# Performance work log

Measured on AMD Instinct MI355X. Metric: run time of the kernel, lower is better.

Reference implementation:

```python
import jax, jax.numpy as jnp
import numpy as np

E = 8           # num_local_experts
H = 1024        # hidden_size
F = 1024        # moe_ffn_hidden_size (per-half; fc1 out = 2*F due to GLU)
T = 16384       # total dispatched tokens
GLU_LINEAR_OFFSET = 1.0


def setup_inputs() -> dict:
    key = jax.random.key(0)
    ks = jax.random.split(key, 7)
    s1 = 1.0 / np.sqrt(H)
    s2 = 1.0 / np.sqrt(F)
    return {
        "hidden_states": jax.random.normal(ks[0], (T, H), jnp.float32),
        "tokens_per_expert": jnp.full((E,), T // E, dtype=jnp.int64),
        "probs": jax.random.uniform(ks[1], (T,), jnp.float32),
        # expert params; torch Linear W is [out,in], stored here as [in,out] (same math)
        "W1": jax.random.uniform(ks[2], (E, H, 2 * F), jnp.float32, -s1, s1),
        "b1": jax.random.uniform(ks[3], (E, 2 * F), jnp.float32, -s1, s1),
        "W2": jax.random.uniform(ks[4], (E, F, H), jnp.float32, -s2, s2),
        "b2": jax.random.uniform(ks[5], (E, H), jnp.float32, -s2, s2),
    }


def reference(hidden_states, tokens_per_expert, probs, W1, b1, W2, b2):
    # Tokens arrive grouped contiguously by expert with equal counts (as in
    # setup_inputs), so the split/loop/cat in the torch module is exactly a
    # reshape + grouped (batched) GEMM over the expert axis.
    e = W1.shape[0]
    t, h = hidden_states.shape
    x = hidden_states.reshape(e, t // e, h)            # [E, Tpe, H]
    p = probs.reshape(e, t // e)                       # [E, Tpe]
    # fc1 (gated)
    y = jnp.einsum('eth,ehf->etf', x, W1) + b1[:, None, :]  # [E, Tpe, 2F]
    gate, lin = jnp.split(y, 2, axis=-1)
    a = jax.nn.silu(gate) * (lin + GLU_LINEAR_OFFSET)       # [E, Tpe, F]
    a = a * p[..., None]                                    # per-token scale
    # fc2
    out = jnp.einsum('etf,efh->eth', a, W2) + b2[:, None, :]
    return out.reshape(t, h)
```

## Files before the change

### kernel.cpp

```cpp
#include <hip/hip_runtime.h>
#include <hip/hip_bf16.h>
#include <stdint.h>

#define T_TOK 16384
#define H_DIM 1024
#define F_DIM 1024
#define E_NUM 8
#define TPE   2048

typedef unsigned short u16;
typedef __attribute__((ext_vector_type(8))) short bf16x8;
typedef __attribute__((ext_vector_type(4))) float f32x4;
typedef __attribute__((ext_vector_type(8))) u16 u16x8;

__device__ __forceinline__ u16 f2bf(float x) {
  unsigned int u = __float_as_uint(x);
  u = (u + 0x7fffu + ((u >> 16) & 1u)) >> 16;
  return (u16)u;
}

#define GLD16(gp, lp)                                                          \
  __builtin_amdgcn_global_load_lds(                                            \
      (const __attribute__((address_space(1))) void*)(gp),                     \
      (__attribute__((address_space(3))) void*)(lp), 16, 0, 0)

__global__ __launch_bounds__(256) void prep_all(
    const float* __restrict__ x, const float* __restrict__ W1,
    const float* __restrict__ W2, u16* __restrict__ xbf,
    u16* __restrict__ w1t, u16* __restrict__ w2t) {
  const int bid = blockIdx.x;
  const int t = threadIdx.x;

  if (bid < 4096) {
    size_t base = (size_t)bid * 4096 + (size_t)t * 16;
    const float4* s = (const float4*)(x + base);
    float4 v0 = s[0], v1 = s[1], v2 = s[2], v3 = s[3];
    u16x8 o0, o1;
    o0[0] = f2bf(v0.x); o0[1] = f2bf(v0.y); o0[2] = f2bf(v0.z); o0[3] = f2bf(v0.w);
    o0[4] = f2bf(v1.x); o0[5] = f2bf(v1.y); o0[6] = f2bf(v1.z); o0[7] = f2bf(v1.w);
    o1[0] = f2bf(v2.x); o1[1] = f2bf(v2.y); o1[2] = f2bf(v2.z); o1[3] = f2bf(v2.w);
    o1[4] = f2bf(v3.x); o1[5] = f2bf(v3.y); o1[6] = f2bf(v3.z); o1[7] = f2bf(v3.w);
    *(u16x8*)(xbf + base) = o0;
    *(u16x8*)(xbf + base + 8) = o1;
    return;
  }

  const float* src; u16* dst; int R, C, gw;
  int e, rc, cc;
  const int lane = t & 63;
  const int wid = t >> 6;
  if (bid < 6144) {
    src = W1; dst = w1t; R = H_DIM; C = 2 * F_DIM;
    gw = (bid - 4096) * 4 + wid;
    e = gw >> 10; int rem = gw & 1023; rc = rem >> 5; cc = rem & 31;
  } else {
    src = W2; dst = w2t; R = F_DIM; C = H_DIM;
    gw = (bid - 6144) * 4 + wid;
    e = gw >> 9; int rem = gw & 511; rc = rem >> 4; cc = rem & 15;
  }
  const int row0 = rc << 5;
  const int col0 = cc << 6;
  const float* s = src + (size_t)e * R * C + (size_t)row0 * C + col0 + lane;
  float v[32];
#pragma unroll
  for (int r = 0; r < 32; ++r) v[r] = s[(size_t)r * C];
  u16* d = dst + (size_t)e * C * R + (size_t)(col0 + lane) * R + row0;
#pragma unroll
  for (int k = 0; k < 4; ++k) {
    u16x8 w;
#pragma unroll
    for (int i = 0; i < 8; ++i) w[i] = f2bf(v[k * 8 + i]);
    *(u16x8*)(d + k * 8) = w;
  }
}


#define DSA2(b, h, ks)                                                         \
  _Pragma("unroll") for (int m2_ = 0; m2_ < 2; ++m2_)                          \
      aF[m2_] = *(const bf16x8*)(sm + (b) * 32768 + aRowBase +                 \
                                 ((h) * 2 + m2_) * 2048 + koff[ks]);

#define DSB4(b, ks)                                                            \
  _Pragma("unroll") for (int n_ = 0; n_ < 4; ++n_)                             \
      bF[n_] = *(const bf16x8*)(sm + 65536 + (b) * 32768 + bRowBase +          \
                                n_ * 2048 + koff[ks]);

#define MFMAP(h)                                                               \
  _Pragma("unroll") for (int n_ = 0; n_ < 4; ++n_)                             \
  _Pragma("unroll") for (int m2_ = 0; m2_ < 2; ++m2_)                          \
      acc[(h) * 2 + m2_][n_] = __builtin_amdgcn_mfma_f32_16x16x32_bf16(        \
          aF[m2_], bF[n_], acc[(h) * 2 + m2_][n_], 0, 0, 0);

#define PF_A(db, q, d) GLD16(aP[q] + (d), sm + (db) * 32768 + (q) * 16384 + tid * 16)
#define PF_B(db, q, d) GLD16(bP[q] + (d), sm + 65536 + (db) * 32768 + (q) * 16384 + tid * 16)

#define VMW(N) asm volatile("s_waitcnt vmcnt(" #N ")" ::: "memory");

#define PHASEK(b, ks, h, PFC, WTC)                                             \
  do {                                                                         \
    DSA2(b, h, ks);                                                            \
    if ((h) == 0) { DSB4(b, ks); }                                             \
    PFC                                                                        \
    __builtin_amdgcn_s_setprio(1);                                             \
    MFMAP(h);                                                                  \
    __builtin_amdgcn_s_setprio(0);                                             \
    WTC                                                                        \
    __builtin_amdgcn_s_barrier();                                              \
  } while (0)

#define KLOOP_BODY                                                             \
  PF_B(0, 0, 0); PF_B(0, 1, 0);                                                \
  PF_A(0, 0, 0); PF_A(0, 1, 0);                                                \
  PF_B(1, 0, 64); PF_B(1, 1, 64);                                              \
  VMW(2)                                                                       \
  __builtin_amdgcn_s_barrier();                                                \
  for (int it = 0; it < 7; ++it) {                                             \
    PHASEK(0, 0, 0, PF_A(1, 0, 64);, );                                        \
    PHASEK(0, 0, 1, PF_A(1, 1, 64);, );                                        \
    PHASEK(0, 1, 0, , );                                                       \
    PHASEK(0, 1, 1, PF_B(0, 0, 128); PF_B(0, 1, 128);, VMW(2));                \
    PHASEK(1, 0, 0, PF_A(0, 0, 128);, );                                       \
    PHASEK(1, 0, 1, PF_A(0, 1, 128);, );                                       \
    PHASEK(1, 1, 0, , );                                                       \
    PHASEK(1, 1, 1, PF_B(1, 0, 192); PF_B(1, 1, 192);, VMW(2));                \
    _Pragma("unroll") for (int q_ = 0; q_ < 2; ++q_) {                         \
      aP[q_] += 128; bP[q_] += 128;                                            \
    }                                                                          \
  }                                                                            \
  PHASEK(0, 0, 0, PF_A(1, 0, 64);, );                                          \
  PHASEK(0, 0, 1, PF_A(1, 1, 64);, );                                          \
  PHASEK(0, 1, 0, , );                                                         \
  PHASEK(0, 1, 1, , VMW(0));                                                   \
  PHASEK(1, 0, 0, , );                                                         \
  PHASEK(1, 0, 1, , );                                                         \
  PHASEK(1, 1, 0, , );                                                         \
  PHASEK(1, 1, 1, , );

__global__ __launch_bounds__(1024) void gemm1_8p(
    const u16* __restrict__ xbf, const u16* __restrict__ w1t,
    const float* __restrict__ b1, const float* __restrict__ probs,
    u16* __restrict__ abf) {
  extern __shared__ char sm[];
  const int tid = threadIdx.x;
  const int lane = tid & 63;
  const int wid = tid >> 6;
  const int wm = wid >> 2, wn = wid & 3;
  const int bid = blockIdx.x;
  const int e = bid & 7;
  const int inner = bid >> 3;
  const int mt = inner >> 3, ct = inner & 7;
  const int tokBase = e * TPE + mt * 256;
  const int c0 = ct * 128;
  const int lrow = lane & 15, lkhi = lane >> 4;

  const u16* aP[2]; const u16* bP[2];
#pragma unroll
  for (int q = 0; q < 2; ++q) {
    int lin = q * 16384 + tid * 16;
    int lg = lin ^ (((lin >> 7) & 7) << 4);
    int row = lg >> 7, kk = (lg & 127) >> 1;
    aP[q] = xbf + (size_t)(tokBase + row) * H_DIM + kk;
    int col = (((row >> 5) & 1) << 10) + c0 + ((row >> 6) << 5) + (row & 31);
    bP[q] = w1t + (size_t)(e * 2 * F_DIM + col) * H_DIM + kk;
  }
  const int aRowBase = (wm * 64 + lrow) * 128;
  const int bRowBase = (wn * 64 + lrow) * 128;
  int koff[2];
#pragma unroll
  for (int ks = 0; ks < 2; ++ks)
    koff[ks] = ((ks << 6) | (lkhi << 4)) ^ ((lane & 7) << 4);

  f32x4 acc[4][4];
#pragma unroll
  for (int i = 0; i < 4; ++i)
#pragma unroll
    for (int j = 0; j < 4; ++j) acc[i][j] = f32x4{0.f, 0.f, 0.f, 0.f};
  bf16x8 aF[2], bF[4];

  KLOOP_BODY

#pragma unroll
  for (int j = 0; j < 2; ++j) {
    int cf = c0 + wn * 32 + j * 16 + lrow;
    float gb = b1[e * 2 * F_DIM + cf];
    float lb = b1[e * 2 * F_DIM + F_DIM + cf];
#pragma unroll
    for (int i = 0; i < 4; ++i) {
      int trow = tokBase + wm * 64 + i * 16 + lkhi * 4;
#pragma unroll
      for (int r = 0; r < 4; ++r) {
        float g = acc[i][j][r] + gb;
        float l = acc[i][j + 2][r] + lb + 1.0f;
        float p = probs[trow + r];
        float sig = 1.0f / (1.0f + __expf(-g));
        abf[(size_t)(trow + r) * F_DIM + cf] = f2bf(g * sig * l * p);
      }
    }
  }
}

__global__ __launch_bounds__(1024) void gemm2_8p(
    const u16* __restrict__ abf, const u16* __restrict__ w2t,
    const float* __restrict__ b2, float* __restrict__ out) {
  extern __shared__ char sm[];
  const int tid = threadIdx.x;
  const int lane = tid & 63;
  const int wid = tid >> 6;
  const int wm = wid >> 2, wn = wid & 3;
  const int bid = blockIdx.x;
  const int e = bid & 7;
  const int inner = bid >> 3;
  const int mt = inner >> 2, nt = inner & 3;
  const int tokBase = e * TPE + mt * 256;
  const int h0 = nt * 256;
  const int lrow = lane & 15, lkhi = lane >> 4;

  const u16* aP[2]; const u16* bP[2];
#pragma unroll
  for (int q = 0; q < 2; ++q) {
    int lin = q * 16384 + tid * 16;
    int lg = lin ^ (((lin >> 7) & 7) << 4);
    int row = lg >> 7, kk = (lg & 127) >> 1;
    aP[q] = abf + (size_t)(tokBase + row) * F_DIM + kk;
    bP[q] = w2t + (size_t)(e * H_DIM + h0 + row) * F_DIM + kk;
  }
  const int aRowBase = (wm * 64 + lrow) * 128;
  const int bRowBase = (wn * 64 + lrow) * 128;
  int koff[2];
#pragma unroll
  for (int ks = 0; ks < 2; ++ks)
    koff[ks] = ((ks << 6) | (lkhi << 4)) ^ ((lane & 7) << 4);

  f32x4 acc[4][4];
#pragma unroll
  for (int i = 0; i < 4; ++i)
#pragma unroll
    for (int j = 0; j < 4; ++j) acc[i][j] = f32x4{0.f, 0.f, 0.f, 0.f};
  bf16x8 aF[2], bF[4];

  KLOOP_BODY

#pragma unroll
  for (int j = 0; j < 4; ++j) {
    int h = h0 + wn * 64 + j * 16 + lrow;
    float bb = b2[e * H_DIM + h];
#pragma unroll
    for (int i = 0; i < 4; ++i) {
      int trow = tokBase + wm * 64 + i * 16 + lkhi * 4;
#pragma unroll
      for (int r = 0; r < 4; ++r)
        out[(size_t)(trow + r) * H_DIM + h] = acc[i][j][r] + bb;
    }
  }
}

extern "C" void kernel_launch(void* const* d_in, const int* in_sizes, int n_in,
                              void* d_out, int out_size, void* d_ws,
                              size_t ws_size, hipStream_t stream) {
  const float* x     = (const float*)d_in[0];
  const float* probs = (const float*)d_in[2];
  const float* W1    = (const float*)d_in[3];
  const float* b1    = (const float*)d_in[4];
  const float* W2    = (const float*)d_in[5];
  const float* b2    = (const float*)d_in[6];
  float* out = (float*)d_out;

  if (ws_size < 117440512u) return;
  char* ws = (char*)d_ws;
  u16* xbf = (u16*)(ws);
  u16* w1t = (u16*)(ws + 33554432);
  u16* w2t = (u16*)(ws + 67108864);
  u16* abf = (u16*)(ws + 83886080);

  (void)hipFuncSetAttribute(reinterpret_cast<const void*>(gemm1_8p),
                            hipFuncAttributeMaxDynamicSharedMemorySize, 131072);
  (void)hipFuncSetAttribute(reinterpret_cast<const void*>(gemm2_8p),
                            hipFuncAttributeMaxDynamicSharedMemorySize, 131072);

  prep_all<<<7168, 256, 0, stream>>>(x, W1, W2, xbf, w1t, w2t);
  gemm1_8p<<<E_NUM * 8 * 8, 1024, 131072, stream>>>(xbf, w1t, b1, probs, abf);
  gemm2_8p<<<E_NUM * 8 * 4, 1024, 131072, stream>>>(abf, w2t, b2, out);
}
```

Baseline: 167.4 us.

## Stage weight transpose through swizzled LDS with async loads, batch x-conversion per block

The prep kernel's weight transpose-and-convert now loads 64x64 fp32 tiles into LDS with global_load_lds, using an XOR swizzle and double buffering. Each block handles four tiles, and the transposed bf16 rows are written as 16-byte vectors. Before, each lane read with a column stride and wrote 16-byte chunks per row. The x conversion now loops four times per block, and the grid shrinks from 7168 to 2560 blocks. The aim is coalesced reads and writes for the transpose and less block launch overhead, at the cost of LDS use and barriers.

Measured after the change: 152.2 us. 1.1x faster.

```diff
diff --git a/kernel.cpp b/kernel.cpp
--- a/kernel.cpp
+++ b/kernel.cpp
@@ -24,54 +24,91 @@
       (const __attribute__((address_space(1))) void*)(gp),                     \
       (__attribute__((address_space(3))) void*)(lp), 16, 0, 0)
 
+#define VMW(N) asm volatile("s_waitcnt vmcnt(" #N ")" ::: "memory");
+
 __global__ __launch_bounds__(256) void prep_all(
     const float* __restrict__ x, const float* __restrict__ W1,
     const float* __restrict__ W2, u16* __restrict__ xbf,
     u16* __restrict__ w1t, u16* __restrict__ w2t) {
+  __shared__ char lds[32768];
   const int bid = blockIdx.x;
   const int t = threadIdx.x;
 
-  if (bid < 4096) {
-    size_t base = (size_t)bid * 4096 + (size_t)t * 16;
-    const float4* s = (const float4*)(x + base);
-    float4 v0 = s[0], v1 = s[1], v2 = s[2], v3 = s[3];
-    u16x8 o0, o1;
-    o0[0] = f2bf(v0.x); o0[1] = f2bf(v0.y); o0[2] = f2bf(v0.z); o0[3] = f2bf(v0.w);
-    o0[4] = f2bf(v1.x); o0[5] = f2bf(v1.y); o0[6] = f2bf(v1.z); o0[7] = f2bf(v1.w);
-    o1[0] = f2bf(v2.x); o1[1] = f2bf(v2.y); o1[2] = f2bf(v2.z); o1[3] = f2bf(v2.w);
-    o1[4] = f2bf(v3.x); o1[5] = f2bf(v3.y); o1[6] = f2bf(v3.z); o1[7] = f2bf(v3.w);
-    *(u16x8*)(xbf + base) = o0;
-    *(u16x8*)(xbf + base + 8) = o1;
+  if (bid < 1024) {
+#pragma unroll
+    for (int it = 0; it < 4; ++it) {
+      size_t base = ((size_t)it * 1024 + bid) * 4096 + (size_t)t * 16;
+      const float4* s = (const float4*)(x + base);
+      float4 v0 = s[0], v1 = s[1], v2 = s[2], v3 = s[3];
+      u16x8 o0, o1;
+      o0[0] = f2bf(v0.x); o0[1] = f2bf(v0.y); o0[2] = f2bf(v0.z); o0[3] = f2bf(v0.w);
+      o0[4] = f2bf(v1.x); o0[5] = f2bf(v1.y); o0[6] = f2bf(v1.z); o0[7] = f2bf(v1.w);
+      o1[0] = f2bf(v2.x); o1[1] = f2bf(v2.y); o1[2] = f2bf(v2.z); o1[3] = f2bf(v2.w);
+      o1[4] = f2bf(v3.x); o1[5] = f2bf(v3.y); o1[6] = f2bf(v3.z); o1[7] = f2bf(v3.w);
+      *(u16x8*)(xbf + base) = o0;
+      *(u16x8*)(xbf + base + 8) = o1;
+    }
     return;
   }
 
-  const float* src; u16* dst; int R, C, gw;
-  int e, rc, cc;
-  const int lane = t & 63;
-  const int wid = t >> 6;
-  if (bid < 6144) {
-    src = W1; dst = w1t; R = H_DIM; C = 2 * F_DIM;
-    gw = (bid - 4096) * 4 + wid;
-    e = gw >> 10; int rem = gw & 1023; rc = rem >> 5; cc = rem & 31;
-  } else {
-    src = W2; dst = w2t; R = F_DIM; C = H_DIM;
-    gw = (bid - 6144) * 4 + wid;
-    e = gw >> 9; int rem = gw & 511; rc = rem >> 4; cc = rem & 15;
-  }
-  const int row0 = rc << 5;
-  const int col0 = cc << 6;
-  const float* s = src + (size_t)e * R * C + (size_t)row0 * C + col0 + lane;
-  float v[32];
-#pragma unroll
-  for (int r = 0; r < 32; ++r) v[r] = s[(size_t)r * C];
-  u16* d = dst + (size_t)e * C * R + (size_t)(col0 + lane) * R + row0;
+  const float* src; u16* dst; int RR, CC, tbase;
+  if (bid < 2048) { src = W1; dst = w1t; RR = H_DIM; CC = 2 * F_DIM; tbase = (bid - 1024) * 4; }
+  else           { src = W2; dst = w2t; RR = F_DIM; CC = H_DIM;     tbase = (bid - 2048) * 4; }
+  const int tilesPerE = (RR >> 6) * (CC >> 6);
+  const int ctn = CC >> 6;
+
+  const float* sb[4]; u16* db[4];
 #pragma unroll
   for (int k = 0; k < 4; ++k) {
-    u16x8 w;
-#pragma unroll
-    for (int i = 0; i < 8; ++i) w[i] = f2bf(v[k * 8 + i]);
-    *(u16x8*)(d + k * 8) = w;
-  }
+    int id = tbase + k;
+    int e = id / tilesPerE, rem = id - e * tilesPerE;
+    int rt = rem / ctn, ct = rem - rt * ctn;
+    sb[k] = src + (size_t)e * RR * CC + (size_t)(rt << 6) * CC + (ct << 6);
+    db[k] = dst + (size_t)e * CC * RR + (size_t)(ct << 6) * RR + (rt << 6);
+  }
+
+#define TSTAGE(buf, k)                                                         \
+  _Pragma("unroll") for (int p_ = 0; p_ < 4; ++p_) {                           \
+    int lin_ = p_ * 4096 + t * 16;                                             \
+    int lg_ = lin_ ^ (((lin_ >> 11) & 7) << 4);                                \
+    int row_ = lg_ >> 8, col_ = (lg_ & 255) >> 2;                              \
+    GLD16(sb[k] + (size_t)row_ * CC + col_, lds + (buf) * 16384 + lin_);       \
+  }
+
+#define TPROC(buf, k)                                                          \
+  _Pragma("unroll") for (int q_ = 0; q_ < 2; ++q_) {                           \
+    int id_ = t + q_ * 256;                                                    \
+    int o_ = id_ >> 3, c_ = id_ & 7;                                           \
+    u16x8 w_;                                                                  \
+    _Pragma("unroll") for (int i_ = 0; i_ < 8; ++i_) {                         \
+      float f_ = *(const float*)(lds + (buf) * 16384 + (c_ * 8 + i_) * 256 +   \
+                                 ((o_ * 4) ^ (c_ << 4)));                      \
+      w_[i_] = f2bf(f_);                                                       \
+    }                                                                          \
+    *(u16x8*)(db[k] + (size_t)o_ * RR + c_ * 8) = w_;                          \
+  }
+
+  TSTAGE(0, 0)
+  TSTAGE(1, 1)
+  VMW(4)
+  __syncthreads();
+  TPROC(0, 0)
+  __syncthreads();
+  TSTAGE(0, 2)
+  VMW(6)
+  __syncthreads();
+  TPROC(1, 1)
+  __syncthreads();
+  TSTAGE(1, 3)
+  VMW(6)
+  __syncthreads();
+  TPROC(0, 2)
+  __syncthreads();
+  VMW(2)
+  __syncthreads();
+  TPROC(1, 3)
+#undef TSTAGE
+#undef TPROC
 }
 
 
@@ -93,8 +130,6 @@
 
 #define PF_A(db, q, d) GLD16(aP[q] + (d), sm + (db) * 32768 + (q) * 16384 + tid * 16)
 #define PF_B(db, q, d) GLD16(bP[q] + (d), sm + 65536 + (db) * 32768 + (q) * 16384 + tid * 16)
-
-#define VMW(N) asm volatile("s_waitcnt vmcnt(" #N ")" ::: "memory");
 
 #define PHASEK(b, ks, h, PFC, WTC)                                             \
   do {                                                                         \
@@ -277,7 +312,7 @@
   (void)hipFuncSetAttribute(reinterpret_cast<const void*>(gemm2_8p),
                             hipFuncAttributeMaxDynamicSharedMemorySize, 131072);
 
-  prep_all<<<7168, 256, 0, stream>>>(x, W1, W2, xbf, w1t, w2t);
+  prep_all<<<2560, 256, 0, stream>>>(x, W1, W2, xbf, w1t, w2t);
   gemm1_8p<<<E_NUM * 8 * 8, 1024, 131072, stream>>>(xbf, w1t, b1, probs, abf);
   gemm2_8p<<<E_NUM * 8 * 4, 1024, 131072, stream>>>(abf, w2t, b2, out);
 }
```
